# Optimization experiments

Measured on AMD Instinct MI355X. Metric: run time of the kernel, lower is better.

## Reference

```python
import jax, jax.numpy as jnp
import numpy as np

N = 50000   # num_nodes
R = 32      # num_relations
D_IN = 128
D_HID = 128
E = 600000  # num_edges
T = 8192    # num scored triplets


def setup_inputs() -> dict:
    key = jax.random.key(0)
    ks = jax.random.split(key, 10)
    return {
        "x_emb": jax.random.normal(ks[0], (N, D_IN), jnp.float32),
        "W": jax.random.normal(ks[1], (R, D_IN, D_HID), jnp.float32) * 0.05,
        "W_root": jax.random.normal(ks[2], (D_IN, D_HID), jnp.float32) * 0.05,
        "bias": jnp.zeros((D_HID,), jnp.float32),
        "rel_emb": jax.random.normal(ks[3], (R, D_HID), jnp.float32),
        "edge_index": jax.random.randint(ks[4], (2, E), 0, N, jnp.int64),
        "edge_type": jax.random.randint(ks[5], (E,), 0, R, jnp.int64),
        "head_idx": jax.random.randint(ks[6], (T,), 0, N, jnp.int64),
        "tail_idx": jax.random.randint(ks[7], (T,), 0, N, jnp.int64),
        "rel_idx": jax.random.randint(ks[8], (T,), 0, R, jnp.int64),
    }


def reference(x_emb, W, W_root, bias, rel_emb,
              edge_index, edge_type, head_idx, tail_idx, rel_idx):
    # --- RGCNConv (PyG semantics: per-relation mean aggregation + root + bias) ---
    src, tgt = edge_index[0], edge_index[1]
    # segment id combining target node and relation: mean is computed per (node, relation)
    seg = tgt * R + edge_type                              # [E]
    ones = jnp.ones((seg.shape[0],), x_emb.dtype)
    cnt = jax.ops.segment_sum(ones, seg, num_segments=N * R)   # [N*R]
    norm = 1.0 / jnp.maximum(cnt[seg], 1.0)                    # [E]
    # Aggregate source features first (W is linear, so transform after aggregation)
    agg = jax.ops.segment_sum(x_emb[src] * norm[:, None], seg, num_segments=N * R)
    agg = agg.reshape(N, R, D_IN)                              # [N, R, d_in]
    h = jnp.einsum('nri,rio->no', agg, W) + x_emb @ W_root + bias  # [N, d_hid]
    h = jax.nn.relu(h)
    # --- DistMult triplet scoring: sum(h * r * t) ---
    scores = jnp.sum(h[head_idx] * rel_emb[rel_idx] * h[tail_idx], axis=-1)  # [T]
    return scores
```

## Files before the change

### kernel.cpp

```cpp
#include <hip/hip_runtime.h>
#include <hip/hip_bf16.h>

typedef unsigned int u32;
typedef unsigned short u16;
typedef short short8 __attribute__((ext_vector_type(8)));
typedef float f32x4 __attribute__((ext_vector_type(4)));

#define R_ 32
#define KEYS_PER_B 2048
#define SORT_STRIDE 1024
#define CAP 16
#define MAXU 16384

static __device__ __forceinline__ u16 f2bf(float f) {
  u32 u = __float_as_uint(f);
  u = (u + 0x7FFFu + ((u >> 16) & 1u)) >> 16;
  return (u16)u;
}
static __device__ __forceinline__ u32 pk2(float a, float b) {
  __hip_bfloat162 h2 = __float22bfloat162_rn(make_float2(a, b));
  union { __hip_bfloat162 h; u32 u; } cv; cv.h = h2; return cv.u;
}

static __device__ __forceinline__ int sort_key(int ct, int r) {
  return (ct >> 6) * KEYS_PER_B + ((ct >> 4) & 3) * 512 + r * 16 + (ct & 15);
}

__global__ __launch_bounds__(256) void k_prep(
    const float* __restrict__ x, const float* __restrict__ W,
    const float* __restrict__ Wroot, u16* __restrict__ xb,
    u16* __restrict__ wp, u16* __restrict__ wrootp,
    const int* __restrict__ head, const int* __restrict__ tail,
    int* __restrict__ flags, int n4, int convNB, int T) {
  __shared__ u32 lds[8192];
  int bx = blockIdx.x;
  const int t = threadIdx.x;
  if (bx < convNB) {
    int i = bx * 256 + t;
    if (i >= n4) return;
    const float4 f = ((const float4*)x)[i];
    u32 lo = (u32)f2bf(f.x) | ((u32)f2bf(f.y) << 16);
    u32 hi = (u32)f2bf(f.z) | ((u32)f2bf(f.w) << 16);
    ((uint2*)xb)[i] = make_uint2(lo, hi);
    return;
  }
  bx -= convNB;
  if (bx < 33) {
    const int rr = bx;
    const float* src = (rr < 32) ? (W + (size_t)rr * (128 * 128)) : Wroot;
#pragma unroll
    for (int k = 0; k < 16; ++k) {
      const int fi = k * 256 + t;
      const float4 f = ((const float4*)src)[fi];
      u32 lo = (u32)f2bf(f.x) | ((u32)f2bf(f.y) << 16);
      u32 hi = (u32)f2bf(f.z) | ((u32)f2bf(f.w) << 16);
      ((uint2*)lds)[fi] = make_uint2(lo, hi);
    }
    __syncthreads();
    const u16* l16 = (const u16*)lds;
#pragma unroll
    for (int p = 0; p < 8; ++p) {
      const int v = p * 256 + t;
      const int lane = v & 63, ks = (v >> 6) & 3, ct = v >> 8;
      const int i0 = ks * 32 + (lane >> 4) * 8;
      const int o  = ct * 16 + (lane & 15);
      u32 w01 = (u32)l16[(i0 + 0) * 128 + o] | ((u32)l16[(i0 + 1) * 128 + o] << 16);
      u32 w23 = (u32)l16[(i0 + 2) * 128 + o] | ((u32)l16[(i0 + 3) * 128 + o] << 16);
      u32 w45 = (u32)l16[(i0 + 4) * 128 + o] | ((u32)l16[(i0 + 5) * 128 + o] << 16);
      u32 w67 = (u32)l16[(i0 + 6) * 128 + o] | ((u32)l16[(i0 + 7) * 128 + o] << 16);
      u16* dst = (rr < 32) ? (wp + ((size_t)((rr * 8 + ct) * 4 + ks) * 64 + lane) * 8)
                           : (wrootp + ((size_t)((ct * 4 + ks) * 64 + lane)) * 8);
      *(uint4*)dst = make_uint4(w01, w23, w45, w67);
    }
    return;
  }
  bx -= 33;
  int i = bx * 256 + t;
  if (i >= 2 * T) return;
  int n = (i < T) ? head[i] : tail[i - T];
  flags[n] = 1;
}

__global__ __launch_bounds__(256) void k_map(const int* __restrict__ flags,
                                             int* __restrict__ map,
                                             int* __restrict__ inv,
                                             int* __restrict__ cnt, int N) {
  int n = blockIdx.x * 256 + threadIdx.x;
  if (n >= N) return;
  if (flags[n]) {
    int c = atomicAdd(cnt, 1);
    map[n] = c;
    inv[c] = n;
  } else {
    map[n] = -1;
  }
}

__global__ void k_hist(const int* __restrict__ ei, const int* __restrict__ et,
                       const int* __restrict__ map, int* __restrict__ hist, int E) {
  int e = blockIdx.x * 256 + threadIdx.x;
  if (e >= E) return;
  int mt = map[ei[E + e]];
  if (mt >= 0) atomicAdd(hist + sort_key(mt, et[e]), 1);
}

__global__ __launch_bounds__(256) void k_scan_local(const int* __restrict__ hist,
                                                    int* __restrict__ offs) {
  __shared__ int wsum[4];
  int b = blockIdx.x, t = threadIdx.x;
  size_t base = (size_t)b * KEYS_PER_B + (size_t)t * 8;
  int4 a = *(const int4*)(hist + base);
  int4 c = *(const int4*)(hist + base + 4);
  int v[8] = {a.x, a.y, a.z, a.w, c.x, c.y, c.z, c.w};
  int s = 0;
#pragma unroll
  for (int i = 0; i < 8; ++i) s += v[i];
  int lane = t & 63, w = t >> 6;
  int x = s;
#pragma unroll
  for (int off = 1; off < 64; off <<= 1) {
    int y = __shfl_up(x, off);
    if (lane >= off) x += y;
  }
  if (lane == 63) wsum[w] = x;
  __syncthreads();
  int wb = 0;
  for (int i = 0; i < w; ++i) wb += wsum[i];
  int ex = wb + x - s;
  int o[8];
#pragma unroll
  for (int i = 0; i < 8; ++i) { o[i] = ex; ex += v[i]; }
  *(int4*)(offs + base) = make_int4(o[0], o[1], o[2], o[3]);
  *(int4*)(offs + base + 4) = make_int4(o[4], o[5], o[6], o[7]);
}

__global__ void k_scatter(const int* __restrict__ ei, const int* __restrict__ et,
                          const int* __restrict__ map,
                          int* __restrict__ offs, u32* __restrict__ sorted, int E) {
  int e = blockIdx.x * 256 + threadIdx.x;
  if (e >= E) return;
  int mt = map[ei[E + e]];
  if (mt < 0) return;
  int src = ei[e];
  int p = atomicAdd(offs + sort_key(mt, et[e]), 1);
  if (p < SORT_STRIDE)
    sorted[(size_t)(mt >> 6) * SORT_STRIDE + p] = (u32)src | ((u32)(mt & 63) << 16);
}

#define PHASE(RR, XV, EVB)                                                     \
  {                                                                            \
    const int r = (RR);                                                        \
    const int Er = __builtin_amdgcn_readlane(eAll, r);                         \
    _Pragma("unroll") for (int rr = 0; rr < 16; ++rr)                          \
        *(u32*)(aggb + (size_t)(w * 16 + rr) * 136 + 2 * lane) = 0;            \
    {                                                                          \
      const int nB = min(Er - sCur, CAP);                                      \
      int curRow = -1, rc = 0;                                                 \
      float v0 = 0.f, v1 = 0.f;                                                \
      _Pragma("unroll") for (int j = 0; j < CAP; ++j) {                        \
        if (j < nB) {                                                          \
          int e = __builtin_amdgcn_readlane((int)(EVB), j);                    \
          int tl = (e >> 16) & 63;                                             \
          if (tl != curRow) {                                                  \
            if (rc > 0) {                                                      \
              float sc = __builtin_amdgcn_rcpf((float)rc);                     \
              *(u32*)(aggb + (size_t)curRow * 136 + 2 * lane) =                \
                  pk2(v0 * sc, v1 * sc);                                       \
            }                                                                  \
            curRow = tl; v0 = 0.f; v1 = 0.f; rc = 0;                           \
          }                                                                    \
          v0 += __uint_as_float((XV)[j] << 16);                                \
          v1 += __uint_as_float((XV)[j] & 0xFFFF0000u);                        \
          ++rc;                                                                \
        }                                                                      \
      }                                                                        \
      for (int p = sCur + CAP; p < Er; ++p) {                                  \
        u32 e = srt[p];                                                        \
        u32 xvv = *(const u32*)(xb + (size_t)(e & 0xFFFFu) * 128 + 2 * lane);  \
        int tl = (int)((e >> 16) & 63);                                        \
        if (tl != curRow) {                                                    \
          if (rc > 0) {                                                        \
            float sc = __builtin_amdgcn_rcpf((float)rc);                       \
            *(u32*)(aggb + (size_t)curRow * 136 + 2 * lane) =                  \
                pk2(v0 * sc, v1 * sc);                                         \
          }                                                                    \
          curRow = tl; v0 = 0.f; v1 = 0.f; rc = 0;                             \
        }                                                                      \
        v0 += __uint_as_float(xvv << 16);                                      \
        v1 += __uint_as_float(xvv & 0xFFFF0000u);                              \
        ++rc;                                                                  \
      }                                                                        \
      if (rc > 0) {                                                            \
        float sc = __builtin_amdgcn_rcpf((float)rc);                           \
        *(u32*)(aggb + (size_t)curRow * 136 + 2 * lane) =                      \
            pk2(v0 * sc, v1 * sc);                                             \
      }                                                                        \
    }                                                                          \
    asm volatile("s_waitcnt lgkmcnt(0)" ::: "memory");                         \
    __builtin_amdgcn_sched_barrier(0);                                         \
    __builtin_amdgcn_s_barrier();                                              \
    __builtin_amdgcn_sched_barrier(0);                                         \
    short8 bfr[4][2];                                                          \
    _Pragma("unroll") for (int ks = 0; ks < 4; ++ks)                           \
      _Pragma("unroll") for (int c = 0; c < 2; ++c)                            \
        bfr[ks][c] = *(const short8*)(wp +                                     \
            ((size_t)(((r * 8 + wct0 + c) * 4 + ks) * 64 + lane)) * 8);        \
    __builtin_amdgcn_sched_barrier(0);                                         \
    if (r + 2 < R_) {                                                          \
      const int sN = __builtin_amdgcn_readlane(eAll, r + 1);                   \
      const int eN = __builtin_amdgcn_readlane(eAll, r + 2);                   \
      (EVB) = ev2;                                                             \
      const int nBn = min(eN - sN, CAP);                                       \
      _Pragma("unroll") for (int j = 0; j < CAP; ++j) {                        \
        if (j < nBn) {                                                         \
          int e = __builtin_amdgcn_readlane((int)(EVB), j);                    \
          (XV)[j] = *(const u32*)(xb + (size_t)(e & 0xFFFF) * 128 + 2 * lane); \
        }                                                                      \
      }                                                                        \
      if (r + 3 < R_) {                                                        \
        int pcn = eN + m;                                                      \
        if (pcn > clampP) pcn = clampP;                                        \
        ev2 = srt[pcn];                                                        \
      }                                                                        \
    }                                                                          \
    _Pragma("unroll") for (int ks = 0; ks < 4; ++ks) {                         \
      const int kb = ks * 32 + q * 8;                                          \
      short8 af[4];                                                            \
      _Pragma("unroll") for (int rt = 0; rt < 4; ++rt)                         \
        af[rt] = *(const short8*)(aggb + (size_t)(rt * 16 + m) * 136 + kb);    \
      _Pragma("unroll") for (int c = 0; c < 2; ++c)                            \
        _Pragma("unroll") for (int rt = 0; rt < 4; ++rt)                       \
          acc[rt][c] = __builtin_amdgcn_mfma_f32_16x16x32_bf16(                \
              af[rt], bfr[ks][c], acc[rt][c], 0, 0, 0);                        \
    }                                                                          \
    asm volatile("s_waitcnt lgkmcnt(0)" ::: "memory");                         \
    __builtin_amdgcn_sched_barrier(0);                                         \
    __builtin_amdgcn_s_barrier();                                              \
    __builtin_amdgcn_sched_barrier(0);                                         \
    sCur = Er;                                                                 \
  }

__global__ __launch_bounds__(256) void k_batch(
    const u16* __restrict__ xb, const u16* __restrict__ wp, const u16* __restrict__ wrootp,
    const float* __restrict__ bias, const u32* __restrict__ sorted,
    const int* __restrict__ offs, const int* __restrict__ inv,
    const int* __restrict__ cnt, float* __restrict__ h) {
  __shared__ u16 aggb[64 * 136];
  const int nUsed = cnt[0];
  const int b = blockIdx.x, t = threadIdx.x;
  const int nb = b * 64;
  if (nb >= nUsed) return;
  const int lane = t & 63, w = t >> 6;
  const int m = lane & 15, q = lane >> 4;
  const int keyBase = b * KEYS_PER_B;
  const int wkBase = keyBase + w * 512;
  const u32* srt = sorted + (size_t)b * SORT_STRIDE;

  const int nEdge = offs[keyBase + KEYS_PER_B - 1];
  const int clampP = (nEdge > 0) ? nEdge - 1 : 0;
  const int eAll = offs[wkBase + (lane & 31) * 16 + 15];
  int sCur = (w == 0) ? 0 : offs[wkBase - 1];

  const int E0 = __builtin_amdgcn_readlane(eAll, 0);
  const int E1 = __builtin_amdgcn_readlane(eAll, 1);

  u32 evBufA, evBufB, ev2;
  u32 xvA[CAP], xvB[CAP];
  {
    int pc = sCur + m;
    if (pc > clampP) pc = clampP;
    evBufA = srt[pc];
  }
  {
    const int nB = min(E0 - sCur, CAP);
#pragma unroll
    for (int j = 0; j < CAP; ++j) {
      if (j < nB) {
        int e = __builtin_amdgcn_readlane((int)evBufA, j);
        xvA[j] = *(const u32*)(xb + (size_t)(e & 0xFFFF) * 128 + 2 * lane);
      }
    }
  }
  {
    int pc = E0 + m;
    if (pc > clampP) pc = clampP;
    evBufB = srt[pc];
  }
  {
    const int nB = min(E1 - E0, CAP);
#pragma unroll
    for (int j = 0; j < CAP; ++j) {
      if (j < nB) {
        int e = __builtin_amdgcn_readlane((int)evBufB, j);
        xvB[j] = *(const u32*)(xb + (size_t)(e & 0xFFFF) * 128 + 2 * lane);
      }
    }
  }
  {
    int pc = E1 + m;
    if (pc > clampP) pc = clampP;
    ev2 = srt[pc];
  }

  const short8 zero8 = {0, 0, 0, 0, 0, 0, 0, 0};
  f32x4 acc[4][2];
#pragma unroll
  for (int rt = 0; rt < 4; ++rt)
#pragma unroll
    for (int c = 0; c < 2; ++c) acc[rt][c] = (f32x4){0.f, 0.f, 0.f, 0.f};
  const int wct0 = w * 2;

  int nodeR[4]; bool vR[4];
#pragma unroll
  for (int rt = 0; rt < 4; ++rt) {
    int crow = nb + rt * 16 + m;
    vR[rt] = crow < nUsed;
    nodeR[rt] = inv[vR[rt] ? crow : (nUsed - 1)];
  }
#pragma unroll
  for (int ks = 0; ks < 4; ++ks) {
    const int kb = ks * 32 + q * 8;
    short8 af[4];
#pragma unroll
    for (int rt = 0; rt < 4; ++rt)
      af[rt] = vR[rt] ? *(const short8*)(xb + (size_t)nodeR[rt] * 128 + kb) : zero8;
#pragma unroll
    for (int c = 0; c < 2; ++c) {
      short8 bf = *(const short8*)(wrootp + ((size_t)(((wct0 + c) * 4 + ks) * 64 + lane)) * 8);
#pragma unroll
      for (int rt = 0; rt < 4; ++rt)
        acc[rt][c] = __builtin_amdgcn_mfma_f32_16x16x32_bf16(af[rt], bf, acc[rt][c], 0, 0, 0);
    }
  }

  for (int r2 = 0; r2 < R_; r2 += 2) {
    PHASE(r2, xvA, evBufA)
    PHASE(r2 + 1, xvB, evBufB)
  }

#pragma unroll
  for (int c = 0; c < 2; ++c) {
    const int col = (wct0 + c) * 16 + m;
    const float bv = bias[col];
#pragma unroll
    for (int rt = 0; rt < 4; ++rt) {
#pragma unroll
      for (int g = 0; g < 4; ++g) {
        const int row = nb + rt * 16 + q * 4 + g;
        if (row < nUsed) {
          float v = acc[rt][c][g] + bv;
          h[(size_t)row * 128 + col] = v > 0.f ? v : 0.f;
        }
      }
    }
  }
}

__global__ void k_score(const float* __restrict__ h, const float* __restrict__ rel_emb,
                        const int* __restrict__ map,
                        const int* __restrict__ head, const int* __restrict__ tail,
                        const int* __restrict__ rel, float* __restrict__ out, int T) {
  int lane = threadIdx.x & 63, w = threadIdx.x >> 6;
  int gid = blockIdx.x * 4 + w;
  if (gid >= T) return;
  const int hr = map[head[gid]];
  const int tr = map[tail[gid]];
  const float2 h2 = *(const float2*)(h + (size_t)hr * 128 + 2 * lane);
  const float2 t2 = *(const float2*)(h + (size_t)tr * 128 + 2 * lane);
  const float2 r2 = *(const float2*)(rel_emb + (size_t)rel[gid] * 128 + 2 * lane);
  float s = h2.x * r2.x * t2.x + h2.y * r2.y * t2.y;
#pragma unroll
  for (int off = 32; off > 0; off >>= 1) s += __shfl_down(s, off);
  if (lane == 0) out[gid] = s;
}

extern "C" void kernel_launch(void* const* d_in, const int* in_sizes, int n_in,
                              void* d_out, int out_size, void* d_ws, size_t ws_size,
                              hipStream_t stream) {
  const float* x     = (const float*)d_in[0];
  const float* W     = (const float*)d_in[1];
  const float* Wroot = (const float*)d_in[2];
  const float* bias  = (const float*)d_in[3];
  const float* relE  = (const float*)d_in[4];
  const int* ei      = (const int*)d_in[5];
  const int* et      = (const int*)d_in[6];
  const int* headI   = (const int*)d_in[7];
  const int* tailI   = (const int*)d_in[8];
  const int* relI    = (const int*)d_in[9];
  float* out = (float*)d_out;

  const int N = in_sizes[0] / 128;
  const int E = in_sizes[6];
  const int T = in_sizes[7];
  const int NB2 = MAXU / 64;
  const int NKEYS2 = NB2 * KEYS_PER_B;

  char* p = (char*)d_ws;
  auto alloc = [&](size_t bytes) -> void* {
    void* r = (void*)p;
    p += (bytes + 255) & ~(size_t)255;
    return r;
  };
  u16* xb     = (u16*)alloc((size_t)N * 128 * 2);
  u16* wp     = (u16*)alloc((size_t)32 * 2048 * 8 * 2);
  u16* wrootp = (u16*)alloc((size_t)2048 * 8 * 2);
  char* z0    = p;
  int* hist   = (int*)alloc((size_t)NKEYS2 * 4);
  int* flags  = (int*)alloc((size_t)N * 4);
  int* cnt    = (int*)alloc(256);
  size_t zBytes = (size_t)(p - z0);
  int* map    = (int*)alloc((size_t)N * 4);
  int* inv    = (int*)alloc((size_t)MAXU * 4);
  int* offs   = (int*)alloc((size_t)NKEYS2 * 4);
  u32* sorted = (u32*)alloc((size_t)NB2 * SORT_STRIDE * 4);
  float* h    = (float*)alloc((size_t)MAXU * 128 * 4);

  const int n4 = N * 128 / 4;
  const int convNB = (n4 + 255) / 256;
  const int markNB = (2 * T + 255) / 256;

  hipMemsetAsync(z0, 0, zBytes, stream);
  k_prep<<<convNB + 33 + markNB, 256, 0, stream>>>(x, W, Wroot, xb, wp, wrootp,
                                                   headI, tailI, flags, n4, convNB, T);
  k_map<<<(N + 255) / 256, 256, 0, stream>>>(flags, map, inv, cnt, N);
  k_hist<<<(E + 255) / 256, 256, 0, stream>>>(ei, et, map, hist, E);
  k_scan_local<<<NB2, 256, 0, stream>>>(hist, offs);
  k_scatter<<<(E + 255) / 256, 256, 0, stream>>>(ei, et, map, offs, sorted, E);
  k_batch<<<NB2, 256, 0, stream>>>(xb, wp, wrootp, bias, sorted, offs, inv, cnt, h);
  k_score<<<(T + 3) / 4, 256, 0, stream>>>(h, relE, map, headI, tailI, relI, out, T);
}
```

Before: 211.2 us.

## Split relation loop across four blocks per node batch and fold map build into prep

The main batch kernel now launches four blocks per 64-node batch, each handling a group of eight relations. Each block writes its partial pre-activation result to a separate copy of h, and the scoring kernel sums the four partials and applies ReLU. The separate flag and map kernels are replaced by a CAS-based unique-node assignment inside the prep kernel, and the histogram is zeroed there too, which removes one launch and a large memset. The split raises block-level parallelism for a kernel that previously had few blocks, at the cost of four times the h writes and more reads in the scoring kernel; the atomic node ordering also becomes nondeterministic.

```diff
diff --git a/kernel.cpp b/kernel.cpp
--- a/kernel.cpp
+++ b/kernel.cpp
@@ -11,6 +11,8 @@
 #define SORT_STRIDE 1024
 #define CAP 16
 #define MAXU 16384
+#define NSPLIT 4
+#define NRG 8
 
 static __device__ __forceinline__ u16 f2bf(float f) {
   u32 u = __float_as_uint(f);
@@ -31,7 +33,8 @@
     const float* __restrict__ Wroot, u16* __restrict__ xb,
     u16* __restrict__ wp, u16* __restrict__ wrootp,
     const int* __restrict__ head, const int* __restrict__ tail,
-    int* __restrict__ flags, int n4, int convNB, int T) {
+    int* __restrict__ map, int* __restrict__ inv, int* __restrict__ cnt,
+    int* __restrict__ hist, int n4, int convNB, int histZB, int T) {
   __shared__ u32 lds[8192];
   int bx = blockIdx.x;
   const int t = threadIdx.x;
@@ -75,24 +78,18 @@
     return;
   }
   bx -= 33;
+  if (bx < histZB) {
+    ((int4*)hist)[bx * 256 + t] = make_int4(0, 0, 0, 0);
+    return;
+  }
+  bx -= histZB;
   int i = bx * 256 + t;
   if (i >= 2 * T) return;
   int n = (i < T) ? head[i] : tail[i - T];
-  flags[n] = 1;
-}
-
-__global__ __launch_bounds__(256) void k_map(const int* __restrict__ flags,
-                                             int* __restrict__ map,
-                                             int* __restrict__ inv,
-                                             int* __restrict__ cnt, int N) {
-  int n = blockIdx.x * 256 + threadIdx.x;
-  if (n >= N) return;
-  if (flags[n]) {
-    int c = atomicAdd(cnt, 1);
+  if (atomicCAS(map + n, -1, -2) == -1) {
+    int c = atomicAdd(cnt, 1) + 1;
+    inv[c] = n;
     map[n] = c;
-    inv[c] = n;
-  } else {
-    map[n] = -1;
   }
 }
 
@@ -147,7 +144,7 @@
     sorted[(size_t)(mt >> 6) * SORT_STRIDE + p] = (u32)src | ((u32)(mt & 63) << 16);
 }
 
-#define PHASE(RR, XV, EVB)                                                     \
+#define PHASE(RR, RI, XV, EVB)                                                 \
   {                                                                            \
     const int r = (RR);                                                        \
     const int Er = __builtin_amdgcn_readlane(eAll, r);                         \
@@ -206,7 +203,7 @@
         bfr[ks][c] = *(const short8*)(wp +                                     \
             ((size_t)(((r * 8 + wct0 + c) * 4 + ks) * 64 + lane)) * 8);        \
     __builtin_amdgcn_sched_barrier(0);                                         \
-    if (r + 2 < R_) {                                                          \
+    if ((RI) + 2 < NRG) {                                                      \
       const int sN = __builtin_amdgcn_readlane(eAll, r + 1);                   \
       const int eN = __builtin_amdgcn_readlane(eAll, r + 2);                   \
       (EVB) = ev2;                                                             \
@@ -217,7 +214,7 @@
           (XV)[j] = *(const u32*)(xb + (size_t)(e & 0xFFFF) * 128 + 2 * lane); \
         }                                                                      \
       }                                                                        \
-      if (r + 3 < R_) {                                                        \
+      if ((RI) + 3 < NRG) {                                                    \
         int pcn = eN + m;                                                      \
         if (pcn > clampP) pcn = clampP;                                        \
         ev2 = srt[pcn];                                                        \
@@ -246,10 +243,13 @@
     const int* __restrict__ offs, const int* __restrict__ inv,
     const int* __restrict__ cnt, float* __restrict__ h) {
   __shared__ u16 aggb[64 * 136];
-  const int nUsed = cnt[0];
-  const int b = blockIdx.x, t = threadIdx.x;
+  const int nUsed = cnt[0] + 1;
+  const int qs = blockIdx.x & (NSPLIT - 1);
+  const int b = blockIdx.x >> 2;
+  const int t = threadIdx.x;
   const int nb = b * 64;
   if (nb >= nUsed) return;
+  const int r0 = qs * NRG;
   const int lane = t & 63, w = t >> 6;
   const int m = lane & 15, q = lane >> 4;
   const int keyBase = b * KEYS_PER_B;
@@ -259,10 +259,10 @@
   const int nEdge = offs[keyBase + KEYS_PER_B - 1];
   const int clampP = (nEdge > 0) ? nEdge - 1 : 0;
   const int eAll = offs[wkBase + (lane & 31) * 16 + 15];
-  int sCur = (w == 0) ? 0 : offs[wkBase - 1];
-
-  const int E0 = __builtin_amdgcn_readlane(eAll, 0);
-  const int E1 = __builtin_amdgcn_readlane(eAll, 1);
+  int sCur = (w == 0 && qs == 0) ? 0 : offs[wkBase + r0 * 16 - 1];
+
+  const int E0 = __builtin_amdgcn_readlane(eAll, r0);
+  const int E1 = __builtin_amdgcn_readlane(eAll, r0 + 1);
 
   u32 evBufA, evBufB, ev2;
   u32 xvA[CAP], xvB[CAP];
@@ -310,47 +310,47 @@
     for (int c = 0; c < 2; ++c) acc[rt][c] = (f32x4){0.f, 0.f, 0.f, 0.f};
   const int wct0 = w * 2;
 
-  int nodeR[4]; bool vR[4];
-#pragma unroll
-  for (int rt = 0; rt < 4; ++rt) {
-    int crow = nb + rt * 16 + m;
-    vR[rt] = crow < nUsed;
-    nodeR[rt] = inv[vR[rt] ? crow : (nUsed - 1)];
-  }
-#pragma unroll
-  for (int ks = 0; ks < 4; ++ks) {
-    const int kb = ks * 32 + q * 8;
-    short8 af[4];
-#pragma unroll
-    for (int rt = 0; rt < 4; ++rt)
-      af[rt] = vR[rt] ? *(const short8*)(xb + (size_t)nodeR[rt] * 128 + kb) : zero8;
-#pragma unroll
-    for (int c = 0; c < 2; ++c) {
-      short8 bf = *(const short8*)(wrootp + ((size_t)(((wct0 + c) * 4 + ks) * 64 + lane)) * 8);
+  if (qs == 0) {
+    int nodeR[4]; bool vR[4];
+#pragma unroll
+    for (int rt = 0; rt < 4; ++rt) {
+      int crow = nb + rt * 16 + m;
+      vR[rt] = crow < nUsed;
+      nodeR[rt] = inv[vR[rt] ? crow : (nUsed - 1)];
+    }
+#pragma unroll
+    for (int ks = 0; ks < 4; ++ks) {
+      const int kb = ks * 32 + q * 8;
+      short8 af[4];
 #pragma unroll
       for (int rt = 0; rt < 4; ++rt)
-        acc[rt][c] = __builtin_amdgcn_mfma_f32_16x16x32_bf16(af[rt], bf, acc[rt][c], 0, 0, 0);
-    }
-  }
-
-  for (int r2 = 0; r2 < R_; r2 += 2) {
-    PHASE(r2, xvA, evBufA)
-    PHASE(r2 + 1, xvB, evBufB)
-  }
-
+        af[rt] = vR[rt] ? *(const short8*)(xb + (size_t)nodeR[rt] * 128 + kb) : zero8;
+#pragma unroll
+      for (int c = 0; c < 2; ++c) {
+        short8 bf = *(const short8*)(wrootp + ((size_t)(((wct0 + c) * 4 + ks) * 64 + lane)) * 8);
+#pragma unroll
+        for (int rt = 0; rt < 4; ++rt)
+          acc[rt][c] = __builtin_amdgcn_mfma_f32_16x16x32_bf16(af[rt], bf, acc[rt][c], 0, 0, 0);
+      }
+    }
+  }
+
+  for (int ri = 0; ri < NRG; ri += 2) {
+    PHASE(r0 + ri, ri, xvA, evBufA)
+    PHASE(r0 + ri + 1, ri + 1, xvB, evBufB)
+  }
+
+  float* hq = h + (size_t)qs * MAXU * 128;
 #pragma unroll
   for (int c = 0; c < 2; ++c) {
     const int col = (wct0 + c) * 16 + m;
-    const float bv = bias[col];
+    const float bv = (qs == 0) ? bias[col] : 0.f;
 #pragma unroll
     for (int rt = 0; rt < 4; ++rt) {
 #pragma unroll
       for (int g = 0; g < 4; ++g) {
         const int row = nb + rt * 16 + q * 4 + g;
-        if (row < nUsed) {
-          float v = acc[rt][c][g] + bv;
-          h[(size_t)row * 128 + col] = v > 0.f ? v : 0.f;
-        }
+        if (row < nUsed) hq[(size_t)row * 128 + col] = acc[rt][c][g] + bv;
       }
     }
   }
@@ -365,10 +365,21 @@
   if (gid >= T) return;
   const int hr = map[head[gid]];
   const int tr = map[tail[gid]];
-  const float2 h2 = *(const float2*)(h + (size_t)hr * 128 + 2 * lane);
-  const float2 t2 = *(const float2*)(h + (size_t)tr * 128 + 2 * lane);
+  const size_t ho = (size_t)hr * 128 + 2 * lane;
+  const size_t to = (size_t)tr * 128 + 2 * lane;
+  float hx = 0.f, hy = 0.f, tx = 0.f, ty = 0.f;
+#pragma unroll
+  for (int s = 0; s < NSPLIT; ++s) {
+    const float2 a = *(const float2*)(h + (size_t)s * (MAXU * 128) + ho);
+    const float2 c = *(const float2*)(h + (size_t)s * (MAXU * 128) + to);
+    hx += a.x; hy += a.y; tx += c.x; ty += c.y;
+  }
+  hx = hx > 0.f ? hx : 0.f;
+  hy = hy > 0.f ? hy : 0.f;
+  tx = tx > 0.f ? tx : 0.f;
+  ty = ty > 0.f ? ty : 0.f;
   const float2 r2 = *(const float2*)(rel_emb + (size_t)rel[gid] * 128 + 2 * lane);
-  float s = h2.x * r2.x * t2.x + h2.y * r2.y * t2.y;
+  float s = hx * r2.x * tx + hy * r2.y * ty;
 #pragma unroll
   for (int off = 32; off > 0; off >>= 1) s += __shfl_down(s, off);
   if (lane == 0) out[gid] = s;
@@ -404,28 +415,26 @@
   u16* xb     = (u16*)alloc((size_t)N * 128 * 2);
   u16* wp     = (u16*)alloc((size_t)32 * 2048 * 8 * 2);
   u16* wrootp = (u16*)alloc((size_t)2048 * 8 * 2);
-  char* z0    = p;
   int* hist   = (int*)alloc((size_t)NKEYS2 * 4);
-  int* flags  = (int*)alloc((size_t)N * 4);
-  int* cnt    = (int*)alloc(256);
-  size_t zBytes = (size_t)(p - z0);
-  int* map    = (int*)alloc((size_t)N * 4);
+  int* map    = (int*)alloc((size_t)(N + 64) * 4);
+  int* cnt    = map + N;
   int* inv    = (int*)alloc((size_t)MAXU * 4);
   int* offs   = (int*)alloc((size_t)NKEYS2 * 4);
   u32* sorted = (u32*)alloc((size_t)NB2 * SORT_STRIDE * 4);
-  float* h    = (float*)alloc((size_t)MAXU * 128 * 4);
+  float* h    = (float*)alloc((size_t)NSPLIT * MAXU * 128 * 4);
 
   const int n4 = N * 128 / 4;
   const int convNB = (n4 + 255) / 256;
+  const int histZB = NKEYS2 / 1024;
   const int markNB = (2 * T + 255) / 256;
 
-  hipMemsetAsync(z0, 0, zBytes, stream);
-  k_prep<<<convNB + 33 + markNB, 256, 0, stream>>>(x, W, Wroot, xb, wp, wrootp,
-                                                   headI, tailI, flags, n4, convNB, T);
-  k_map<<<(N + 255) / 256, 256, 0, stream>>>(flags, map, inv, cnt, N);
+  hipMemsetAsync(map, 0xFF, (size_t)(N + 64) * 4, stream);
+  k_prep<<<convNB + 33 + histZB + markNB, 256, 0, stream>>>(
+      x, W, Wroot, xb, wp, wrootp, headI, tailI, map, inv, cnt, hist,
+      n4, convNB, histZB, T);
   k_hist<<<(E + 255) / 256, 256, 0, stream>>>(ei, et, map, hist, E);
   k_scan_local<<<NB2, 256, 0, stream>>>(hist, offs);
   k_scatter<<<(E + 255) / 256, 256, 0, stream>>>(ei, et, map, offs, sorted, E);
-  k_batch<<<NB2, 256, 0, stream>>>(xb, wp, wrootp, bias, sorted, offs, inv, cnt, h);
+  k_batch<<<NB2 * NSPLIT, 256, 0, stream>>>(xb, wp, wrootp, bias, sorted, offs, inv, cnt, h);
   k_score<<<(T + 3) / 4, 256, 0, stream>>>(h, relE, map, headI, tailI, relI, out, T);
 }
```

New measurement: 188.8 us. 1.12x faster.
